# Optimization experiments

Hardware: AMD Instinct MI355X
Metric: run time of the kernel (lower is better)

The kernel has to match this reference:

```python
import jax, jax.numpy as jnp
import numpy as np

GAMMA = 0.99
CLIP_VALUE = 5.0
B, T = 4096, 2048


def setup_inputs() -> dict:
    key = jax.random.key(0)
    k1, k2, k3, k4 = jax.random.split(key, 4)
    return {
        "log_probs": jax.random.normal(k1, (B, T), dtype=jnp.float32),
        "logits": jax.random.normal(k2, (B, T, 1), dtype=jnp.float32),
        "weight": jax.random.uniform(k3, (B, T), dtype=jnp.float32),
        "baselines": jax.random.normal(k4, (B, T, 1), dtype=jnp.float32),
    }


def _discounted_cumulative(wr, gamma):
    # wr: [B, T]. cum[t] = sum_{s>=t} gamma^(s-t) * wr[s]
    # Reverse-time linear recurrence: c[t] = wr[t] + gamma * c[t+1]
    def step(c, x):
        c = x + gamma * c
        return c, c
    # scan over time in reverse; xs laid out time-major [T, B]
    _, cum_rev = jax.lax.scan(step, jnp.zeros(wr.shape[0], wr.dtype), wr[:, ::-1].T)
    return cum_rev[::-1].T  # back to [B, T]


def reference(log_probs, logits, weight, baselines):
    rewards = jax.nn.log_sigmoid(logits[..., 0])          # [B, T]
    cumulative_rewards = _discounted_cumulative(weight * rewards, GAMMA)  # [B, T]
    advantages = cumulative_rewards - baselines[..., 0]
    advantages = advantages - advantages.mean(axis=0)      # center over batch
    advantages = jnp.clip(advantages, -CLIP_VALUE, CLIP_VALUE)
    generator_objective = (advantages * log_probs).sum(axis=0)  # [T]
    return (generator_objective, cumulative_rewards)
```

## Files before the change

### kernel.cpp

```cpp
#include <hip/hip_runtime.h>
#include <math.h>

#define BDIM 4096
#define TDIM 2048
#define NBLK 512
#define RPB  8

constexpr double gpow(int e) {
    double r = 1.0;
    for (int i = 0; i < e; ++i) r *= 0.99;
    return r;
}

__device__ __forceinline__ float logsig_fast(float x) {
    float z = __expf(-fabsf(x));
    return fminf(x, 0.0f) - __logf(1.0f + z);
}

__device__ __forceinline__ float clip5(float x) {
    return fminf(fmaxf(x, -5.0f), 5.0f);
}

__global__ __launch_bounds__(256) void k1_scan(
    const float* __restrict__ logits,
    const float* __restrict__ weight,
    const float* __restrict__ baselines,
    float* __restrict__ cum_out,
    float* __restrict__ partial,
    float* __restrict__ colsum,
    float* __restrict__ obj)
{
    const int tid  = threadIdx.x;
    const int lane = tid & 63;
    const int wave = tid >> 6;
    const int t0   = tid * 8;

    if (blockIdx.x == 0) {
        *reinterpret_cast<float4*>(colsum + t0)     = make_float4(0.f, 0.f, 0.f, 0.f);
        *reinterpret_cast<float4*>(colsum + t0 + 4) = make_float4(0.f, 0.f, 0.f, 0.f);
    }
    if (blockIdx.x == 1) {
        *reinterpret_cast<float4*>(obj + t0)     = make_float4(0.f, 0.f, 0.f, 0.f);
        *reinterpret_cast<float4*>(obj + t0 + 4) = make_float4(0.f, 0.f, 0.f, 0.f);
    }

    const float G    = 0.99f;
    const float G512 = (float)gpow(512);
    const float LOG2G = -0.014499569695115089f;
    const float gk[8] = {(float)gpow(8), (float)gpow(7), (float)gpow(6), (float)gpow(5),
                         (float)gpow(4), (float)gpow(3), (float)gpow(2), (float)gpow(1)};
    const float fs[6] = {(float)gpow(8),  (float)gpow(16), (float)gpow(32),
                         (float)gpow(64), (float)gpow(128), (float)gpow(256)};
    const float lane_pow = exp2f((float)((64 - lane) * 8) * LOG2G);

    __shared__ float wsum[2][4];

    float colacc[8];
#pragma unroll
    for (int k = 0; k < 8; ++k) colacc[k] = 0.0f;

    const int row0 = blockIdx.x * RPB;
    size_t base = (size_t)row0 * TDIM + t0;

    float4 x0 = *reinterpret_cast<const float4*>(logits + base);
    float4 x1 = *reinterpret_cast<const float4*>(logits + base + 4);
    float4 w0 = *reinterpret_cast<const float4*>(weight + base);
    float4 w1 = *reinterpret_cast<const float4*>(weight + base + 4);
    float4 b0 = *reinterpret_cast<const float4*>(baselines + base);
    float4 b1 = *reinterpret_cast<const float4*>(baselines + base + 4);

    for (int r = 0; r < RPB; ++r) {
        const size_t nbase = base + TDIM;
        const bool has_next = (r + 1 < RPB);

        float wr[8];
        wr[0] = w0.x * logsig_fast(x0.x); wr[1] = w0.y * logsig_fast(x0.y);
        wr[2] = w0.z * logsig_fast(x0.z); wr[3] = w0.w * logsig_fast(x0.w);
        wr[4] = w1.x * logsig_fast(x1.x); wr[5] = w1.y * logsig_fast(x1.y);
        wr[6] = w1.z * logsig_fast(x1.z); wr[7] = w1.w * logsig_fast(x1.w);

        float4 nx0, nx1, nw0, nw1, nb0, nb1;
        if (has_next) {
            nx0 = *reinterpret_cast<const float4*>(logits + nbase);
            nx1 = *reinterpret_cast<const float4*>(logits + nbase + 4);
            nw0 = *reinterpret_cast<const float4*>(weight + nbase);
            nw1 = *reinterpret_cast<const float4*>(weight + nbase + 4);
            nb0 = *reinterpret_cast<const float4*>(baselines + nbase);
            nb1 = *reinterpret_cast<const float4*>(baselines + nbase + 4);
        }

        float loc[8];
        loc[7] = wr[7];
#pragma unroll
        for (int k = 6; k >= 0; --k) loc[k] = fmaf(G, loc[k + 1], wr[k]);

        float v = loc[0];
#pragma unroll
        for (int s = 0; s < 6; ++s) {
            const int o = 1 << s;
            float up = __shfl_down(v, (unsigned)o, 64);
            if (lane + o < 64) v = fmaf(fs[s], up, v);
        }

        const int buf = r & 1;
        if (lane == 0) wsum[buf][wave] = v;
        __syncthreads();
        const float W1 = wsum[buf][1], W2 = wsum[buf][2], W3 = wsum[buf][3];
        const float FC3 = W3;
        const float FC2 = fmaf(G512, FC3, W2);
        const float FC1 = fmaf(G512, FC2, W1);
        const float carry = (wave == 0) ? FC1 : (wave == 1) ? FC2 : (wave == 2) ? FC3 : 0.0f;

        const float vfull = fmaf(lane_pow, carry, v);
        const float vn = __shfl_down(vfull, 1, 64);
        const float tail = (lane == 63) ? carry : vn;

        float c[8];
#pragma unroll
        for (int k = 0; k < 8; ++k) c[k] = fmaf(gk[k], tail, loc[k]);

        *reinterpret_cast<float4*>(cum_out + base)     = make_float4(c[0], c[1], c[2], c[3]);
        *reinterpret_cast<float4*>(cum_out + base + 4) = make_float4(c[4], c[5], c[6], c[7]);

        colacc[0] += c[0] - b0.x; colacc[1] += c[1] - b0.y;
        colacc[2] += c[2] - b0.z; colacc[3] += c[3] - b0.w;
        colacc[4] += c[4] - b1.x; colacc[5] += c[5] - b1.y;
        colacc[6] += c[6] - b1.z; colacc[7] += c[7] - b1.w;

        base = nbase;
        if (has_next) {
            x0 = nx0; x1 = nx1; w0 = nw0; w1 = nw1; b0 = nb0; b1 = nb1;
        }
    }

    const size_t pbase = (size_t)blockIdx.x * TDIM + t0;
    *reinterpret_cast<float4*>(partial + pbase)     = make_float4(colacc[0], colacc[1], colacc[2], colacc[3]);
    *reinterpret_cast<float4*>(partial + pbase + 4) = make_float4(colacc[4], colacc[5], colacc[6], colacc[7]);
}

__global__ __launch_bounds__(256) void k2_colsum(
    const float* __restrict__ partial, float* __restrict__ colsum)
{
    const int gid = blockIdx.x * 256 + threadIdx.x;
    const int col = gid & (TDIM - 1);
    const int slc = gid >> 11;
    const float* p = partial + (size_t)slc * 16 * TDIM + col;
    float s = 0.0f;
#pragma unroll
    for (int i = 0; i < 16; ++i) s += p[(size_t)i * TDIM];
    atomicAdd(colsum + col, s);
}

#define K3_ROWS 32
__global__ __launch_bounds__(256) void k3_obj(
    const float* __restrict__ cum,
    const float* __restrict__ baselines,
    const float* __restrict__ lp,
    const float* __restrict__ colsum,
    float* __restrict__ obj)
{
    const int c4 = (blockIdx.x * 256 + threadIdx.x) * 4;
    const int r0 = blockIdx.y * K3_ROWS;
    const float inv = 1.0f / (float)BDIM;
    float4 ms = *reinterpret_cast<const float4*>(colsum + c4);
    const float m0 = ms.x * inv, m1 = ms.y * inv, m2 = ms.z * inv, m3 = ms.w * inv;

    float a0 = 0.0f, a1 = 0.0f, a2 = 0.0f, a3 = 0.0f;
    size_t idx = (size_t)r0 * TDIM + c4;
#pragma unroll 8
    for (int r = 0; r < K3_ROWS; ++r, idx += TDIM) {
        float4 c = *reinterpret_cast<const float4*>(cum + idx);
        float4 b = *reinterpret_cast<const float4*>(baselines + idx);
        float4 l = *reinterpret_cast<const float4*>(lp + idx);
        a0 = fmaf(clip5(c.x - b.x - m0), l.x, a0);
        a1 = fmaf(clip5(c.y - b.y - m1), l.y, a1);
        a2 = fmaf(clip5(c.z - b.z - m2), l.z, a2);
        a3 = fmaf(clip5(c.w - b.w - m3), l.w, a3);
    }
    atomicAdd(obj + c4 + 0, a0);
    atomicAdd(obj + c4 + 1, a1);
    atomicAdd(obj + c4 + 2, a2);
    atomicAdd(obj + c4 + 3, a3);
}

extern "C" void kernel_launch(void* const* d_in, const int* in_sizes, int n_in,
                              void* d_out, int out_size, void* d_ws, size_t ws_size,
                              hipStream_t stream) {
    const float* log_probs = (const float*)d_in[0];
    const float* logits    = (const float*)d_in[1];
    const float* weight    = (const float*)d_in[2];
    const float* baselines = (const float*)d_in[3];

    float* out = (float*)d_out;
    float* obj = out;
    float* cum = out + TDIM;

    float* partial = (float*)d_ws;
    float* colsum  = partial + (size_t)NBLK * TDIM;

    k1_scan<<<NBLK, 256, 0, stream>>>(logits, weight, baselines, cum, partial, colsum, obj);
    k2_colsum<<<256, 256, 0, stream>>>(partial, colsum);
    k3_obj<<<dim3(TDIM / (256 * 4), BDIM / K3_ROWS), 256, 0, stream>>>(
        cum, baselines, log_probs, colsum, obj);
}
```

Measured before the change: 181.7 us.

## Process four rows concurrently per scan block and shrink k3 row tiles

The scan kernel now launches 1024-thread blocks with four 256-thread groups, each handling a different row in parallel (2 rows per group instead of 8 sequential rows per block). Per-group column partials are merged through shared memory before being written out. This is meant to cut the serial row-loop latency and raise memory-level parallelism. The cost is extra shared memory and block-wide barriers that couple all groups. Separately, k3 uses 16 rows per block instead of 32, which doubles the grid and the number of atomics.

Result: slower. 186.9 us (+2.9%).

```diff
diff --git a/kernel.cpp b/kernel.cpp
--- a/kernel.cpp
+++ b/kernel.cpp
@@ -5,6 +5,7 @@
 #define TDIM 2048
 #define NBLK 512
 #define RPB  8
+#define GROUPS 4
 
 constexpr double gpow(int e) {
     double r = 1.0;
@@ -21,7 +22,7 @@
     return fminf(fmaxf(x, -5.0f), 5.0f);
 }
 
-__global__ __launch_bounds__(256) void k1_scan(
+__global__ __launch_bounds__(1024, 8) void k1_scan(
     const float* __restrict__ logits,
     const float* __restrict__ weight,
     const float* __restrict__ baselines,
@@ -30,16 +31,18 @@
     float* __restrict__ colsum,
     float* __restrict__ obj)
 {
-    const int tid  = threadIdx.x;
-    const int lane = tid & 63;
-    const int wave = tid >> 6;
-    const int t0   = tid * 8;
-
-    if (blockIdx.x == 0) {
+    const int tid    = threadIdx.x;
+    const int group  = tid >> 8;
+    const int gt     = tid & 255;
+    const int lane   = tid & 63;
+    const int wavein = (tid >> 6) & 3;
+    const int t0     = gt * 8;
+
+    if (blockIdx.x == 0 && tid < 256) {
         *reinterpret_cast<float4*>(colsum + t0)     = make_float4(0.f, 0.f, 0.f, 0.f);
         *reinterpret_cast<float4*>(colsum + t0 + 4) = make_float4(0.f, 0.f, 0.f, 0.f);
     }
-    if (blockIdx.x == 1) {
+    if (blockIdx.x == 1 && tid < 256) {
         *reinterpret_cast<float4*>(obj + t0)     = make_float4(0.f, 0.f, 0.f, 0.f);
         *reinterpret_cast<float4*>(obj + t0 + 4) = make_float4(0.f, 0.f, 0.f, 0.f);
     }
@@ -53,14 +56,15 @@
                          (float)gpow(64), (float)gpow(128), (float)gpow(256)};
     const float lane_pow = exp2f((float)((64 - lane) * 8) * LOG2G);
 
-    __shared__ float wsum[2][4];
+    __shared__ float wsum[GROUPS][2][4];
+    __shared__ float merge[3][256][8];
 
     float colacc[8];
 #pragma unroll
     for (int k = 0; k < 8; ++k) colacc[k] = 0.0f;
 
     const int row0 = blockIdx.x * RPB;
-    size_t base = (size_t)row0 * TDIM + t0;
+    size_t base = (size_t)(row0 + group) * TDIM + t0;
 
     float4 x0 = *reinterpret_cast<const float4*>(logits + base);
     float4 x1 = *reinterpret_cast<const float4*>(logits + base + 4);
@@ -69,9 +73,10 @@
     float4 b0 = *reinterpret_cast<const float4*>(baselines + base);
     float4 b1 = *reinterpret_cast<const float4*>(baselines + base + 4);
 
-    for (int r = 0; r < RPB; ++r) {
-        const size_t nbase = base + TDIM;
-        const bool has_next = (r + 1 < RPB);
+#pragma unroll
+    for (int i = 0; i < 2; ++i) {
+        const size_t nbase = base + (size_t)GROUPS * TDIM;
+        const bool has_next = (i == 0);
 
         float wr[8];
         wr[0] = w0.x * logsig_fast(x0.x); wr[1] = w0.y * logsig_fast(x0.y);
@@ -102,14 +107,13 @@
             if (lane + o < 64) v = fmaf(fs[s], up, v);
         }
 
-        const int buf = r & 1;
-        if (lane == 0) wsum[buf][wave] = v;
+        if (lane == 0) wsum[group][i][wavein] = v;
         __syncthreads();
-        const float W1 = wsum[buf][1], W2 = wsum[buf][2], W3 = wsum[buf][3];
+        const float W1 = wsum[group][i][1], W2 = wsum[group][i][2], W3 = wsum[group][i][3];
         const float FC3 = W3;
         const float FC2 = fmaf(G512, FC3, W2);
         const float FC1 = fmaf(G512, FC2, W1);
-        const float carry = (wave == 0) ? FC1 : (wave == 1) ? FC2 : (wave == 2) ? FC3 : 0.0f;
+        const float carry = (wavein == 0) ? FC1 : (wavein == 1) ? FC2 : (wavein == 2) ? FC3 : 0.0f;
 
         const float vfull = fmaf(lane_pow, carry, v);
         const float vn = __shfl_down(vfull, 1, 64);
@@ -133,9 +137,25 @@
         }
     }
 
-    const size_t pbase = (size_t)blockIdx.x * TDIM + t0;
-    *reinterpret_cast<float4*>(partial + pbase)     = make_float4(colacc[0], colacc[1], colacc[2], colacc[3]);
-    *reinterpret_cast<float4*>(partial + pbase + 4) = make_float4(colacc[4], colacc[5], colacc[6], colacc[7]);
+    if (group != 0) {
+        *reinterpret_cast<float4*>(&merge[group - 1][gt][0]) =
+            make_float4(colacc[0], colacc[1], colacc[2], colacc[3]);
+        *reinterpret_cast<float4*>(&merge[group - 1][gt][4]) =
+            make_float4(colacc[4], colacc[5], colacc[6], colacc[7]);
+    }
+    __syncthreads();
+    if (group == 0) {
+#pragma unroll
+        for (int g = 0; g < 3; ++g) {
+            float4 m0 = *reinterpret_cast<const float4*>(&merge[g][gt][0]);
+            float4 m1 = *reinterpret_cast<const float4*>(&merge[g][gt][4]);
+            colacc[0] += m0.x; colacc[1] += m0.y; colacc[2] += m0.z; colacc[3] += m0.w;
+            colacc[4] += m1.x; colacc[5] += m1.y; colacc[6] += m1.z; colacc[7] += m1.w;
+        }
+        const size_t pbase = (size_t)blockIdx.x * TDIM + t0;
+        *reinterpret_cast<float4*>(partial + pbase)     = make_float4(colacc[0], colacc[1], colacc[2], colacc[3]);
+        *reinterpret_cast<float4*>(partial + pbase + 4) = make_float4(colacc[4], colacc[5], colacc[6], colacc[7]);
+    }
 }
 
 __global__ __launch_bounds__(256) void k2_colsum(
@@ -151,7 +171,7 @@
     atomicAdd(colsum + col, s);
 }
 
-#define K3_ROWS 32
+#define K3_ROWS 16
 __global__ __launch_bounds__(256) void k3_obj(
     const float* __restrict__ cum,
     const float* __restrict__ baselines,
@@ -167,7 +187,7 @@
 
     float a0 = 0.0f, a1 = 0.0f, a2 = 0.0f, a3 = 0.0f;
     size_t idx = (size_t)r0 * TDIM + c4;
-#pragma unroll 8
+#pragma unroll 4
     for (int r = 0; r < K3_ROWS; ++r, idx += TDIM) {
         float4 c = *reinterpret_cast<const float4*>(cum + idx);
         float4 b = *reinterpret_cast<const float4*>(baselines + idx);
@@ -198,7 +218,7 @@
     float* partial = (float*)d_ws;
     float* colsum  = partial + (size_t)NBLK * TDIM;
 
-    k1_scan<<<NBLK, 256, 0, stream>>>(logits, weight, baselines, cum, partial, colsum, obj);
+    k1_scan<<<NBLK, 1024, 0, stream>>>(logits, weight, baselines, cum, partial, colsum, obj);
     k2_colsum<<<256, 256, 0, stream>>>(partial, colsum);
     k3_obj<<<dim3(TDIM / (256 * 4), BDIM / K3_ROWS), 256, 0, stream>>>(
         cum, baselines, log_probs, colsum, obj);
```
